# Optimization experiments

Measured on AMD Instinct MI355X. Metric: run time of the kernel, lower is better.

## Reference

```python
import jax, jax.numpy as jnp
import numpy as np

NUM_CP = 16
DEGREE = 3
START = -3.0
END = 3.0
GRID_SIZE = 1000


def _compute_basis_grid(n, k, start, end, grid_size):
    # Cox-de Boor recursion evaluated on a dense grid (numpy, done once at setup).
    knots = np.linspace(start, end, n + k + 1).astype(np.float64)
    x = np.linspace(start, end, grid_size).astype(np.float64)[:, None]  # [G,1]
    basis = ((x >= knots[:-1]) & (x < knots[1:])).astype(np.float64)    # [G, n+k]
    basis[:, -1] = np.where(x[:, 0] == knots[-1], 1.0, basis[:, -1])
    eps = 1e-10
    for deg in range(1, k + 1):
        nb = n + k - deg
        k_i = knots[:nb]
        k_i_deg = knots[deg:deg + nb]
        k_i1 = knots[1:nb + 1]
        k_i1_deg = knots[deg + 1:deg + nb + 1]
        d1 = k_i_deg - k_i
        d2 = k_i1_deg - k_i1
        w1 = np.where(np.abs(d1) > eps, (x - k_i) / np.where(np.abs(d1) > eps, d1, 1.0), 0.0)
        w2 = np.where(np.abs(d2) > eps, (k_i1_deg - x) / np.where(np.abs(d2) > eps, d2, 1.0), 0.0)
        basis = w1 * basis[:, :nb] + w2 * basis[:, 1:nb + 1]
    return basis[:, :n].astype(np.float32)  # [G, n]


def setup_inputs() -> dict:
    key = jax.random.key(0)
    kx, = jax.random.split(key, 1)
    x = jax.random.normal(kx, (8, 2048, 1024), dtype=jnp.float32)
    # init='relu': control points = relu(linspace(start, end, n))
    grid_cp = jnp.linspace(START, END, NUM_CP, dtype=jnp.float32)
    control_points = jnp.where(grid_cp >= 0, grid_cp, 0.0)
    basis_grid = jnp.asarray(_compute_basis_grid(NUM_CP, DEGREE, START, END, GRID_SIZE))
    return {"x": x, "control_points": control_points, "basis_grid": basis_grid}


def reference(x, control_points, basis_grid):
    gs = GRID_SIZE
    x_flat = x.reshape(-1)
    x_clamped = jnp.clip(x_flat, START, END)
    ind = (x_clamped - START) / (END - START) * (gs - 1)            # float index into grid
    ind_floor = jnp.clip(jnp.floor(ind).astype(jnp.int32), 0, gs - 1)
    ind_ceil = jnp.clip(ind_floor + 1, 0, gs - 1)
    weight = ind - ind_floor.astype(x_flat.dtype)                   # [N]
    basis_floor = basis_grid[ind_floor]                             # [N, n] gather
    basis_ceil = basis_grid[ind_ceil]                               # [N, n] gather
    basis_interp = basis_floor + weight[:, None] * (basis_ceil - basis_floor)
    out = basis_interp @ control_points                             # [N]
    return out.reshape(x.shape)
```

## Files before the change

kernel.cpp:

```cpp
#include <hip/hip_runtime.h>

#define GS 1000
#define NCP 16
#define XSTART -3.0f
#define XEND 3.0f

__global__ __launch_bounds__(256) void bspline_lut_kernel(
    const float* __restrict__ x,
    const float* __restrict__ cp,
    const float* __restrict__ bg,
    float* __restrict__ out,
    int n4)
{
    __shared__ float tbl[GS];
    for (int i = threadIdx.x; i < GS; i += 256) {
        const float* row = bg + i * NCP;
        float s = 0.0f;
        #pragma unroll
        for (int j = 0; j < NCP; ++j) s += row[j] * cp[j];
        tbl[i] = s;
    }
    __syncthreads();

    const float scale = (float)(GS - 1) / (XEND - XSTART);
    int idx = blockIdx.x * blockDim.x + threadIdx.x;
    int stride = gridDim.x * blockDim.x;

    for (int i = idx; i < n4; i += stride) {
        float4 v = reinterpret_cast<const float4*>(x)[i];
        float vv[4] = {v.x, v.y, v.z, v.w};
        float r[4];
        #pragma unroll
        for (int j = 0; j < 4; ++j) {
            float xc = fminf(fmaxf(vv[j], XSTART), XEND);
            float ind = (xc - XSTART) * scale;
            int f = (int)ind;
            f = min(f, GS - 1);
            int c = min(f + 1, GS - 1);
            float w = ind - (float)f;
            float gf = tbl[f];
            float gc = tbl[c];
            r[j] = gf + w * (gc - gf);
        }
        float4 o = make_float4(r[0], r[1], r[2], r[3]);
        reinterpret_cast<float4*>(out)[i] = o;
    }
}

extern "C" void kernel_launch(void* const* d_in, const int* in_sizes, int n_in,
                              void* d_out, int out_size, void* d_ws, size_t ws_size,
                              hipStream_t stream) {
    const float* x  = (const float*)d_in[0];
    const float* cp = (const float*)d_in[1];
    const float* bg = (const float*)d_in[2];
    float* out = (float*)d_out;

    int n = in_sizes[0];
    int n4 = n / 4;

    int blocks = (n4 + 255) / 256;
    if (blocks > 2048) blocks = 2048;

    bspline_lut_kernel<<<blocks, 256, 0, stream>>>(x, cp, bg, out, n4);
}
```

Measured before the change: 30.97 us.

## Precompute paired LUT in a separate kernel and copy it into shared memory

```diff
diff --git a/kernel.cpp b/kernel.cpp
--- a/kernel.cpp
+++ b/kernel.cpp
@@ -4,6 +4,90 @@
 #define NCP 16
 #define XSTART -3.0f
 #define XEND 3.0f
+
+__device__ __forceinline__ float dot16(const float* __restrict__ row,
+                                       float4 c0, float4 c1, float4 c2, float4 c3) {
+    const float4* r4 = reinterpret_cast<const float4*>(row);
+    float4 a0 = r4[0], a1 = r4[1], a2 = r4[2], a3 = r4[3];
+    float s = a0.x * c0.x;
+    s = fmaf(a0.y, c0.y, s); s = fmaf(a0.z, c0.z, s); s = fmaf(a0.w, c0.w, s);
+    s = fmaf(a1.x, c1.x, s); s = fmaf(a1.y, c1.y, s); s = fmaf(a1.z, c1.z, s); s = fmaf(a1.w, c1.w, s);
+    s = fmaf(a2.x, c2.x, s); s = fmaf(a2.y, c2.y, s); s = fmaf(a2.z, c2.z, s); s = fmaf(a2.w, c2.w, s);
+    s = fmaf(a3.x, c3.x, s); s = fmaf(a3.y, c3.y, s); s = fmaf(a3.z, c3.z, s); s = fmaf(a3.w, c3.w, s);
+    return s;
+}
+
+__global__ __launch_bounds__(256) void build_table_kernel(
+    const float* __restrict__ cp,
+    const float* __restrict__ bg,
+    float2* __restrict__ ws2)
+{
+    int i = blockIdx.x * 256 + threadIdx.x;
+    if (i >= GS) return;
+    const float4* c4 = reinterpret_cast<const float4*>(cp);
+    float4 c0 = c4[0], c1 = c4[1], c2 = c4[2], c3 = c4[3];
+    int i1 = min(i + 1, GS - 1);
+    float g0 = dot16(bg + i * NCP, c0, c1, c2, c3);
+    float g1 = dot16(bg + i1 * NCP, c0, c1, c2, c3);
+    ws2[i] = make_float2(g0, g1);
+}
+
+__device__ __forceinline__ float bspline_eval(float v, const float2* tbl, float scale) {
+    float xc = fminf(fmaxf(v, XSTART), XEND);
+    float ind = (xc - XSTART) * scale;
+    int f = (int)ind;
+    f = min(f, GS - 1);
+    float w = ind - (float)f;
+    float2 p = tbl[f];
+    return fmaf(w, p.y - p.x, p.x);
+}
+
+__global__ __launch_bounds__(256) void bspline_main_kernel(
+    const float* __restrict__ x,
+    const float2* __restrict__ ws2,
+    float* __restrict__ out,
+    int n4)
+{
+    __shared__ float2 tbl[GS];
+    {
+        const float4* src = reinterpret_cast<const float4*>(ws2);
+        float4* dst = reinterpret_cast<float4*>(tbl);
+        for (int i = threadIdx.x; i < GS / 2; i += 256) dst[i] = src[i];
+    }
+    __syncthreads();
+
+    const float scale = (float)(GS - 1) / (XEND - XSTART);
+    const float4* x4 = reinterpret_cast<const float4*>(x);
+    float4* o4 = reinterpret_cast<float4*>(out);
+    int idx = blockIdx.x * 256 + threadIdx.x;
+    int stride = gridDim.x * 256;
+
+    int i = idx;
+    for (; i + stride < n4; i += 2 * stride) {
+        float4 va = x4[i];
+        float4 vb = x4[i + stride];
+        float4 oa, ob;
+        oa.x = bspline_eval(va.x, tbl, scale);
+        oa.y = bspline_eval(va.y, tbl, scale);
+        oa.z = bspline_eval(va.z, tbl, scale);
+        oa.w = bspline_eval(va.w, tbl, scale);
+        ob.x = bspline_eval(vb.x, tbl, scale);
+        ob.y = bspline_eval(vb.y, tbl, scale);
+        ob.z = bspline_eval(vb.z, tbl, scale);
+        ob.w = bspline_eval(vb.w, tbl, scale);
+        o4[i] = oa;
+        o4[i + stride] = ob;
+    }
+    if (i < n4) {
+        float4 va = x4[i];
+        float4 oa;
+        oa.x = bspline_eval(va.x, tbl, scale);
+        oa.y = bspline_eval(va.y, tbl, scale);
+        oa.z = bspline_eval(va.z, tbl, scale);
+        oa.w = bspline_eval(va.w, tbl, scale);
+        o4[i] = oa;
+    }
+}
 
 __global__ __launch_bounds__(256) void bspline_lut_kernel(
     const float* __restrict__ x,
@@ -12,6 +96,7 @@
     float* __restrict__ out,
     int n4)
 {
+    __shared__ float tblس[1];
     __shared__ float tbl[GS];
     for (int i = threadIdx.x; i < GS; i += 256) {
         const float* row = bg + i * NCP;
@@ -21,11 +106,9 @@
         tbl[i] = s;
     }
     __syncthreads();
-
     const float scale = (float)(GS - 1) / (XEND - XSTART);
     int idx = blockIdx.x * blockDim.x + threadIdx.x;
     int stride = gridDim.x * blockDim.x;
-
     for (int i = idx; i < n4; i += stride) {
         float4 v = reinterpret_cast<const float4*>(x)[i];
         float vv[4] = {v.x, v.y, v.z, v.w};
@@ -38,12 +121,9 @@
             f = min(f, GS - 1);
             int c = min(f + 1, GS - 1);
             float w = ind - (float)f;
-            float gf = tbl[f];
-            float gc = tbl[c];
-            r[j] = gf + w * (gc - gf);
+            r[j] = tbl[f] + w * (tbl[c] - tbl[f]);
         }
-        float4 o = make_float4(r[0], r[1], r[2], r[3]);
-        reinterpret_cast<float4*>(out)[i] = o;
+        reinterpret_cast<float4*>(out)[i] = make_float4(r[0], r[1], r[2], r[3]);
     }
 }
 
@@ -61,5 +141,11 @@
     int blocks = (n4 + 255) / 256;
     if (blocks > 2048) blocks = 2048;
 
-    bspline_lut_kernel<<<blocks, 256, 0, stream>>>(x, cp, bg, out, n4);
+    if (ws_size >= GS * sizeof(float2)) {
+        float2* ws2 = (float2*)d_ws;
+        build_table_kernel<<<(GS + 255) / 256, 256, 0, stream>>>(cp, bg, ws2);
+        bspline_main_kernel<<<blocks, 256, 0, stream>>>(x, ws2, out, n4);
+    } else {
+        bspline_lut_kernel<<<blocks, 256, 0, stream>>>(x, cp, bg, out, n4);
+    }
 }
```

Measured after the change: 30.64 us. About the same (-1.0%).

## Precompute paired LUT in separate kernel, prefetch x before table load

Applied to the files above, without the earlier changes.

```diff
diff --git a/kernel.cpp b/kernel.cpp
--- a/kernel.cpp
+++ b/kernel.cpp
@@ -2,8 +2,112 @@
 
 #define GS 1000
 #define NCP 16
-#define XSTART -3.0f
-#define XEND 3.0f
+
+typedef float f32x4 __attribute__((ext_vector_type(4)));
+typedef float f32x2 __attribute__((ext_vector_type(2)));
+
+__device__ __forceinline__ float dot16(const float* __restrict__ row,
+                                       f32x4 c0, f32x4 c1, f32x4 c2, f32x4 c3) {
+    const f32x4* r4 = reinterpret_cast<const f32x4*>(row);
+    f32x4 a0 = r4[0], a1 = r4[1], a2 = r4[2], a3 = r4[3];
+    float s = a0.x * c0.x;
+    s = fmaf(a0.y, c0.y, s); s = fmaf(a0.z, c0.z, s); s = fmaf(a0.w, c0.w, s);
+    s = fmaf(a1.x, c1.x, s); s = fmaf(a1.y, c1.y, s); s = fmaf(a1.z, c1.z, s); s = fmaf(a1.w, c1.w, s);
+    s = fmaf(a2.x, c2.x, s); s = fmaf(a2.y, c2.y, s); s = fmaf(a2.z, c2.z, s); s = fmaf(a2.w, c2.w, s);
+    s = fmaf(a3.x, c3.x, s); s = fmaf(a3.y, c3.y, s); s = fmaf(a3.z, c3.z, s); s = fmaf(a3.w, c3.w, s);
+    return s;
+}
+
+__global__ __launch_bounds__(256) void build_table_kernel(
+    const float* __restrict__ cp,
+    const float* __restrict__ bg,
+    f32x2* __restrict__ ws2)
+{
+    int i = blockIdx.x * 256 + threadIdx.x;
+    if (i >= GS) return;
+    const f32x4* c4 = reinterpret_cast<const f32x4*>(cp);
+    f32x4 c0 = c4[0], c1 = c4[1], c2 = c4[2], c3 = c4[3];
+    int i1 = min(i + 1, GS - 1);
+    float g0 = dot16(bg + i * NCP, c0, c1, c2, c3);
+    float g1 = dot16(bg + i1 * NCP, c0, c1, c2, c3);
+    f32x2 p; p.x = g0; p.y = g1;
+    ws2[i] = p;
+}
+
+__device__ __forceinline__ float evalone(float v, const f32x2* __restrict__ tbl) {
+    float ind = fmaf(v, 166.5f, 499.5f);
+    ind = fminf(fmaxf(ind, 0.0f), 999.0f);
+    float fl = truncf(ind);
+    float w  = ind - fl;
+    f32x2 p = tbl[(int)fl];
+    return fmaf(w, p.y - p.x, p.x);
+}
+
+__device__ __forceinline__ f32x4 eval4(f32x4 v, const f32x2* __restrict__ tbl) {
+    f32x4 r;
+    r.x = evalone(v.x, tbl);
+    r.y = evalone(v.y, tbl);
+    r.z = evalone(v.z, tbl);
+    r.w = evalone(v.w, tbl);
+    return r;
+}
+
+__global__ __launch_bounds__(256) void bspline_main_kernel(
+    const float* __restrict__ x,
+    const f32x2* __restrict__ ws2,
+    float* __restrict__ out,
+    int n4)
+{
+    __shared__ f32x2 tbl[GS];
+    const int tid = threadIdx.x;
+    const int stride = gridDim.x * 256;
+    const f32x4* __restrict__ x4 = reinterpret_cast<const f32x4*>(x);
+    f32x4* __restrict__ o4 = reinterpret_cast<f32x4*>(out);
+
+    int i = blockIdx.x * 256 + tid;
+
+    bool full = (i + 3 * stride < n4);
+    f32x4 a, b, c, d;
+    if (full) {
+        a = x4[i];
+        b = x4[i + stride];
+        c = x4[i + 2 * stride];
+        d = x4[i + 3 * stride];
+    }
+
+    {
+        const f32x4* __restrict__ src = reinterpret_cast<const f32x4*>(ws2);
+        f32x4* dst = reinterpret_cast<f32x4*>(tbl);
+        dst[tid] = src[tid];
+        if (tid < GS / 2 - 256) dst[256 + tid] = src[256 + tid];
+    }
+    __syncthreads();
+
+    while (full) {
+        f32x4 ra = eval4(a, tbl);
+        f32x4 rb = eval4(b, tbl);
+        f32x4 rc = eval4(c, tbl);
+        f32x4 rd = eval4(d, tbl);
+        int ni = i + 4 * stride;
+        bool nfull = (ni + 3 * stride < n4);
+        if (nfull) {
+            a = x4[ni];
+            b = x4[ni + stride];
+            c = x4[ni + 2 * stride];
+            d = x4[ni + 3 * stride];
+        }
+        __builtin_nontemporal_store(ra, &o4[i]);
+        __builtin_nontemporal_store(rb, &o4[i + stride]);
+        __builtin_nontemporal_store(rc, &o4[i + 2 * stride]);
+        __builtin_nontemporal_store(rd, &o4[i + 3 * stride]);
+        i = ni;
+        full = nfull;
+    }
+    for (; i < n4; i += stride) {
+        f32x4 v = x4[i];
+        __builtin_nontemporal_store(eval4(v, tbl), &o4[i]);
+    }
+}
 
 __global__ __launch_bounds__(256) void bspline_lut_kernel(
     const float* __restrict__ x,
@@ -21,29 +125,22 @@
         tbl[i] = s;
     }
     __syncthreads();
-
-    const float scale = (float)(GS - 1) / (XEND - XSTART);
     int idx = blockIdx.x * blockDim.x + threadIdx.x;
     int stride = gridDim.x * blockDim.x;
-
     for (int i = idx; i < n4; i += stride) {
-        float4 v = reinterpret_cast<const float4*>(x)[i];
-        float vv[4] = {v.x, v.y, v.z, v.w};
-        float r[4];
+        f32x4 v = reinterpret_cast<const f32x4*>(x)[i];
+        f32x4 r;
         #pragma unroll
         for (int j = 0; j < 4; ++j) {
-            float xc = fminf(fmaxf(vv[j], XSTART), XEND);
-            float ind = (xc - XSTART) * scale;
-            int f = (int)ind;
-            f = min(f, GS - 1);
-            int c = min(f + 1, GS - 1);
-            float w = ind - (float)f;
-            float gf = tbl[f];
-            float gc = tbl[c];
-            r[j] = gf + w * (gc - gf);
+            float ind = fmaf(v[j], 166.5f, 499.5f);
+            ind = fminf(fmaxf(ind, 0.0f), 999.0f);
+            float fl = truncf(ind);
+            float w  = ind - fl;
+            int f = (int)fl;
+            int cc = min(f + 1, GS - 1);
+            r[j] = fmaf(w, tbl[cc] - tbl[f], tbl[f]);
         }
-        float4 o = make_float4(r[0], r[1], r[2], r[3]);
-        reinterpret_cast<float4*>(out)[i] = o;
+        reinterpret_cast<f32x4*>(out)[i] = r;
     }
 }
 
@@ -61,5 +158,11 @@
     int blocks = (n4 + 255) / 256;
     if (blocks > 2048) blocks = 2048;
 
-    bspline_lut_kernel<<<blocks, 256, 0, stream>>>(x, cp, bg, out, n4);
+    if (ws_size >= GS * sizeof(f32x2)) {
+        f32x2* ws2 = (f32x2*)d_ws;
+        build_table_kernel<<<(GS + 255) / 256, 256, 0, stream>>>(cp, bg, ws2);
+        bspline_main_kernel<<<blocks, 256, 0, stream>>>(x, ws2, out, n4);
+    } else {
+        bspline_lut_kernel<<<blocks, 256, 0, stream>>>(x, cp, bg, out, n4);
+    }
 }
```

Result: no change. 31.13 us (+0.5%).
